# Performance work log

Measured on AMD Instinct MI355X. Metric: run time of the kernel, lower is better.

## Reference

```python
import jax, jax.numpy as jnp
import numpy as np

EMBED_DIM = 1024
NUM_HEADS = 16
HEAD_DIM = EMBED_DIM // NUM_HEADS


def setup_inputs() -> dict:
    key = jax.random.key(0)
    ks = jax.random.split(key, 5)
    B, N, C = 4, 2048, EMBED_DIM
    x = jax.random.normal(ks[0], (B, N, C), dtype=jnp.float32)
    # Linear params (PyTorch layout: weight [out, in])
    s = 1.0 / np.sqrt(C)
    W_qkv = jax.random.uniform(ks[1], (3 * C, C), dtype=jnp.float32, minval=-s, maxval=s)
    b_qkv = jax.random.uniform(ks[2], (3 * C,), dtype=jnp.float32, minval=-s, maxval=s)
    W_out = jax.random.uniform(ks[3], (C, C), dtype=jnp.float32, minval=-s, maxval=s)
    b_out = jax.random.uniform(ks[4], (C,), dtype=jnp.float32, minval=-s, maxval=s)
    return {"x": x, "W_qkv": W_qkv, "b_qkv": b_qkv, "W_out": W_out, "b_out": b_out}


def _rotate_half(t):
    t1, t2 = jnp.split(t, 2, axis=-1)
    return jnp.concatenate((-t2, t1), axis=-1)


def _rope_cos_sin(seq_len, dim, dtype):
    inv_freq = 1.0 / (10000.0 ** (jnp.arange(0, dim, 2, dtype=jnp.float32) / dim))
    t = jnp.arange(seq_len, dtype=jnp.float32)
    freqs = jnp.einsum("i,j->ij", t, inv_freq)  # [N, dim/2]
    emb = jnp.concatenate((freqs, freqs), axis=-1)  # [N, dim]
    return emb.astype(dtype)


def reference(x, W_qkv, b_qkv, W_out, b_out):
    B, N, C = x.shape
    H, D = NUM_HEADS, HEAD_DIM
    qkv = x @ W_qkv.T + b_qkv  # [B, N, 3C]
    qkv = qkv.reshape(B, N, 3, H, D).transpose(2, 0, 3, 1, 4)  # [3, B, H, N, D]
    q, k, v = qkv[0], qkv[1], qkv[2]
    emb = _rope_cos_sin(N, D, x.dtype)
    cos = jnp.cos(emb)[None, None, :, :]  # [1,1,N,D]
    sin = jnp.sin(emb)[None, None, :, :]
    q = q * cos + _rotate_half(q) * sin
    k = k * cos + _rotate_half(k) * sin
    scale = D ** -0.5
    attn = jnp.einsum("bhnd,bhmd->bhnm", q, k) * scale  # [B,H,N,N]
    attn = jax.nn.softmax(attn, axis=-1)
    out = jnp.einsum("bhnm,bhmd->bhnd", attn, v)  # [B,H,N,D]
    out = out.transpose(0, 2, 1, 3).reshape(B, N, C)
    return out @ W_out.T + b_out
```

## Files before the change

### kernel.cpp

```cpp
#include <hip/hip_runtime.h>
#include <hip/hip_bf16.h>
#include <cstdint>
#include <cstddef>

#define SEQ 2048
#define NBATCH 4
#define EMB 1024
#define NH 16
#define HD 64
#define MTOT (NBATCH * SEQ)

typedef __attribute__((ext_vector_type(8))) short bf16x8;
typedef __attribute__((ext_vector_type(4))) float f32x4;
typedef __attribute__((ext_vector_type(16))) float f32x16;
typedef unsigned short u16;
typedef unsigned int u32;

__device__ __forceinline__ float bf2f(u16 v) {
  union { u32 u; float f; } c; c.u = ((u32)v) << 16; return c.f;
}
__device__ __forceinline__ u16 f2bf(float f) {
  union { float f; u32 u; } c; c.f = f;
  u32 u = c.u;
  return (u16)((u + 0x7FFFu + ((u >> 16) & 1u)) >> 16);
}

__global__ void cast_kernel(const float* __restrict__ in, u16* __restrict__ out, int n4) {
  int stride = gridDim.x * blockDim.x;
  for (int i = blockIdx.x * blockDim.x + threadIdx.x; i < n4; i += stride) {
    float4 v = reinterpret_cast<const float4*>(in)[i];
    ushort4 o;
    o.x = f2bf(v.x); o.y = f2bf(v.y); o.z = f2bf(v.z); o.w = f2bf(v.w);
    reinterpret_cast<ushort4*>(out)[i] = o;
  }
}

__global__ void rope_table_kernel(float* __restrict__ tab) {
  int i = blockIdx.x * blockDim.x + threadIdx.x;
  if (i >= SEQ * 32) return;
  int n = i >> 5, j = i & 31;
  float invf = 1.0f / powf(10000.0f, (float)(2 * j) / 64.0f);
  float ang = (float)n * invf;
  tab[i] = cosf(ang);
  tab[SEQ * 32 + i] = sinf(ang);
}

__device__ __forceinline__ void gld_lds16(const u16* g, u16* l) {
  __builtin_amdgcn_global_load_lds((const __attribute__((address_space(1))) void*)g,
                                   (__attribute__((address_space(3))) void*)l, 16, 0, 0);
}

template<bool OUT_F32>
__global__ __launch_bounds__(256, 2)
void gemm_bt(const u16* __restrict__ A, const u16* __restrict__ Bw,
             const float* __restrict__ bias, void* __restrict__ Cout,
             int N, int tiles_n) {
  __shared__ u16 lA[128 * 64];
  __shared__ u16 lB[128 * 64];
  const int K = 1024;
  int bm = blockIdx.x / tiles_n;
  int bn = blockIdx.x % tiles_n;
  int t = threadIdx.x;
  int wave = t >> 6, lane = t & 63;
  int wm = wave >> 1, wn = wave & 1;
  int l15 = lane & 15, l4 = lane >> 4;

  f32x4 acc[4][4];
#pragma unroll
  for (int i = 0; i < 4; ++i)
#pragma unroll
    for (int j = 0; j < 4; ++j) acc[i][j] = (f32x4){0.f, 0.f, 0.f, 0.f};

  int su[4], sr[4], sc[4];
#pragma unroll
  for (int i = 0; i < 4; ++i) {
    int u = (i * 4 + wave) * 64 + lane;
    su[i] = u;
    sr[i] = u >> 3;
    sc[i] = (u & 7) ^ (sr[i] & 7);
  }

  for (int kt = 0; kt < K / 64; ++kt) {
    if (kt) __syncthreads();
#pragma unroll
    for (int i = 0; i < 4; ++i) {
      gld_lds16(A + (size_t)(bm * 128 + sr[i]) * K + kt * 64 + sc[i] * 8, &lA[su[i] * 8]);
      gld_lds16(Bw + (size_t)(bn * 128 + sr[i]) * K + kt * 64 + sc[i] * 8, &lB[su[i] * 8]);
    }
    __syncthreads();
#pragma unroll
    for (int ks = 0; ks < 2; ++ks) {
      bf16x8 af[4], bfr[4];
#pragma unroll
      for (int mb = 0; mb < 4; ++mb) {
        int r = wm * 64 + mb * 16 + l15;
        int cc = (ks * 4 + l4) ^ (r & 7);
        af[mb] = *reinterpret_cast<const bf16x8*>(&lA[r * 64 + cc * 8]);
      }
#pragma unroll
      for (int nb = 0; nb < 4; ++nb) {
        int r = wn * 64 + nb * 16 + l15;
        int cc = (ks * 4 + l4) ^ (r & 7);
        bfr[nb] = *reinterpret_cast<const bf16x8*>(&lB[r * 64 + cc * 8]);
      }
#pragma unroll
      for (int mb = 0; mb < 4; ++mb)
#pragma unroll
        for (int nb = 0; nb < 4; ++nb)
          acc[mb][nb] = __builtin_amdgcn_mfma_f32_16x16x32_bf16(af[mb], bfr[nb], acc[mb][nb], 0, 0, 0);
    }
  }

#pragma unroll
  for (int mb = 0; mb < 4; ++mb)
#pragma unroll
    for (int nb = 0; nb < 4; ++nb) {
      int row0 = bm * 128 + wm * 64 + mb * 16 + l4 * 4;
      int col = bn * 128 + wn * 64 + nb * 16 + l15;
      float bv = bias[col];
#pragma unroll
      for (int r = 0; r < 4; ++r) {
        float v = acc[mb][nb][r] + bv;
        if (OUT_F32)
          reinterpret_cast<float*>(Cout)[(size_t)(row0 + r) * N + col] = v;
        else
          reinterpret_cast<u16*>(Cout)[(size_t)(row0 + r) * N + col] = f2bf(v);
      }
    }
}

__global__ __launch_bounds__(256)
void rope_scatter(const u16* __restrict__ qkv, const float* __restrict__ tab,
                  u16* __restrict__ Q, u16* __restrict__ Kk, u16* __restrict__ Vt) {
  int blk = blockIdx.x;
  int bh = blk >> 5;
  int nt = blk & 31;
  int b = bh >> 4, h = bh & 15;
  int t = threadIdx.x;
  __shared__ u16 vtile[64][72];
  const float* ct = tab;
  const float* st = tab + SEQ * 32;
#pragma unroll
  for (int p = 0; p < 2; ++p) {
    int u = p * 256 + t;
    int r = u >> 3, g = u & 7;
    int n = nt * 64 + r;
    size_t base = (size_t)(b * SEQ + n) * 3072;
    int d0 = g * 8;
    int f0 = d0 & 31;
    bf16x8 qv = *reinterpret_cast<const bf16x8*>(&qkv[base + h * 64 + d0]);
    bf16x8 qp = *reinterpret_cast<const bf16x8*>(&qkv[base + h * 64 + (d0 ^ 32)]);
    bf16x8 kv = *reinterpret_cast<const bf16x8*>(&qkv[base + 1024 + h * 64 + d0]);
    bf16x8 kp = *reinterpret_cast<const bf16x8*>(&qkv[base + 1024 + h * 64 + (d0 ^ 32)]);
    bf16x8 vv = *reinterpret_cast<const bf16x8*>(&qkv[base + 2048 + h * 64 + d0]);
    float4 c0 = *reinterpret_cast<const float4*>(&ct[n * 32 + f0]);
    float4 c1 = *reinterpret_cast<const float4*>(&ct[n * 32 + f0 + 4]);
    float4 s0 = *reinterpret_cast<const float4*>(&st[n * 32 + f0]);
    float4 s1 = *reinterpret_cast<const float4*>(&st[n * 32 + f0 + 4]);
    float sgn = (d0 < 32) ? -1.0f : 1.0f;
    float cs[8] = {c0.x, c0.y, c0.z, c0.w, c1.x, c1.y, c1.z, c1.w};
    float sn[8] = {s0.x, s0.y, s0.z, s0.w, s1.x, s1.y, s1.z, s1.w};
    bf16x8 qo, ko;
#pragma unroll
    for (int j = 0; j < 8; ++j) {
      float qr = bf2f((u16)qv[j]) * cs[j] + sgn * bf2f((u16)qp[j]) * sn[j];
      float kr = bf2f((u16)kv[j]) * cs[j] + sgn * bf2f((u16)kp[j]) * sn[j];
      qo[j] = (short)f2bf(qr * 0.1803368801111163f);
      ko[j] = (short)f2bf(kr);
      vtile[d0 + j][r] = (u16)vv[j];
    }
    size_t qbase = ((size_t)bh * SEQ + n) * 64 + d0;
    *reinterpret_cast<bf16x8*>(&Q[qbase]) = qo;
    *reinterpret_cast<bf16x8*>(&Kk[qbase]) = ko;
  }
  __syncthreads();
#pragma unroll
  for (int p = 0; p < 2; ++p) {
    int u = p * 256 + t;
    int d = u >> 3, c = u & 7;
    bf16x8 o = *reinterpret_cast<const bf16x8*>(&vtile[d][c * 8]);
    *reinterpret_cast<bf16x8*>(&Vt[((size_t)bh * 64 + d) * SEQ + nt * 64 + c * 8]) = o;
  }
}

__global__ __launch_bounds__(256, 2)
void attn_kernel(const u16* __restrict__ Q, const u16* __restrict__ Kk,
                 const u16* __restrict__ Vt, u16* __restrict__ Out) {
  int bid = blockIdx.x;
  int swz = (bid & 7) * 64 + (bid >> 3);
  int bh = swz >> 3;
  int qt = swz & 7;
  int b = bh >> 4, h = bh & 15;
  int t = threadIdx.x;
  int wave = t >> 6, lane = t & 63;
  int l31 = lane & 31, hi = lane >> 5;

  __shared__ u16 lK[2][64 * 64];
  __shared__ u16 lV[2][64 * 64];

  const u16* Qh = Q + (size_t)bh * SEQ * 64;
  const u16* Kh = Kk + (size_t)bh * SEQ * 64;
  const u16* Vh = Vt + (size_t)bh * 64 * SEQ;
  int q0w = qt * 256 + wave * 64;

  bf16x8 qf[2][4];
#pragma unroll
  for (int qb = 0; qb < 2; ++qb)
#pragma unroll
    for (int dc = 0; dc < 4; ++dc)
      qf[qb][dc] = *reinterpret_cast<const bf16x8*>(
          &Qh[(size_t)(q0w + qb * 32 + l31) * 64 + dc * 16 + hi * 8]);

  f32x16 oacc[2][2];
#pragma unroll
  for (int qb = 0; qb < 2; ++qb)
#pragma unroll
    for (int db = 0; db < 2; ++db)
#pragma unroll
      for (int r = 0; r < 16; ++r) oacc[qb][db][r] = 0.f;
  float dn[2] = {0.f, 0.f};

  auto stage = [&](int buf, int kt) {
#pragma unroll
    for (int p = 0; p < 2; ++p) {
      int u = p * 256 + t;
      int r = u >> 3;
      int c = (u & 7) ^ (r & 7);
      gld_lds16(Kh + (size_t)(kt * 64 + r) * 64 + c * 8, &lK[buf][u * 8]);
      gld_lds16(Vh + (size_t)r * SEQ + kt * 64 + c * 8, &lV[buf][u * 8]);
    }
  };

  union PF { u32 w[4]; bf16x8 v; };
  int cur = 0;
  stage(0, 0);
  for (int kt = 0; kt < SEQ / 64; ++kt) {
    if (kt + 1 < SEQ / 64) {
      stage(cur ^ 1, kt + 1);
      asm volatile("s_waitcnt vmcnt(4)" ::: "memory");
    } else {
      asm volatile("s_waitcnt vmcnt(0)" ::: "memory");
    }
    __builtin_amdgcn_s_barrier();

    f32x16 s[2][2];
#pragma unroll
    for (int qb = 0; qb < 2; ++qb)
#pragma unroll
      for (int cb = 0; cb < 2; ++cb)
#pragma unroll
        for (int r = 0; r < 16; ++r) s[qb][cb][r] = 0.f;
#pragma unroll
    for (int cb = 0; cb < 2; ++cb) {
      int krow = cb * 32 + l31;
#pragma unroll
      for (int dc = 0; dc < 4; ++dc) {
        int ch = (dc * 2 + hi) ^ (l31 & 7);
        bf16x8 kf = *reinterpret_cast<const bf16x8*>(&lK[cur][krow * 64 + ch * 8]);
        s[0][cb] = __builtin_amdgcn_mfma_f32_32x32x16_bf16(kf, qf[0][dc], s[0][cb], 0, 0, 0);
        s[1][cb] = __builtin_amdgcn_mfma_f32_32x32x16_bf16(kf, qf[1][dc], s[1][cb], 0, 0, 0);
      }
    }

    PF pa[2][2][2];
#pragma unroll
    for (int qb = 0; qb < 2; ++qb)
#pragma unroll
      for (int cb = 0; cb < 2; ++cb) {
#pragma unroll
        for (int r = 0; r < 16; ++r) {
          float e = __builtin_amdgcn_exp2f(s[qb][cb][r]);
          s[qb][cb][r] = e;
          dn[qb] += e;
        }
#pragma unroll
        for (int c = 0; c < 2; ++c) {
          u32 a1, a2, b1, b2;
          asm("v_cvt_pk_bf16_f32 %0, %1, %2" : "=v"(a1) : "v"(s[qb][cb][8 * c + 0]), "v"(s[qb][cb][8 * c + 1]));
          asm("v_cvt_pk_bf16_f32 %0, %1, %2" : "=v"(a2) : "v"(s[qb][cb][8 * c + 2]), "v"(s[qb][cb][8 * c + 3]));
          asm("v_cvt_pk_bf16_f32 %0, %1, %2" : "=v"(b1) : "v"(s[qb][cb][8 * c + 4]), "v"(s[qb][cb][8 * c + 5]));
          asm("v_cvt_pk_bf16_f32 %0, %1, %2" : "=v"(b2) : "v"(s[qb][cb][8 * c + 6]), "v"(s[qb][cb][8 * c + 7]));
          asm("v_permlane32_swap_b32 %0, %1" : "+v"(a1), "+v"(b1));
          asm("v_permlane32_swap_b32 %0, %1" : "+v"(a2), "+v"(b2));
          pa[qb][cb][c].w[0] = a1; pa[qb][cb][c].w[1] = a2;
          pa[qb][cb][c].w[2] = b1; pa[qb][cb][c].w[3] = b2;
        }
      }

#pragma unroll
    for (int cb = 0; cb < 2; ++cb)
#pragma unroll
      for (int c = 0; c < 2; ++c)
#pragma unroll
        for (int db = 0; db < 2; ++db) {
          int vrow = db * 32 + l31;
          int ch = (cb * 4 + c * 2 + hi) ^ (l31 & 7);
          bf16x8 vf = *reinterpret_cast<const bf16x8*>(&lV[cur][vrow * 64 + ch * 8]);
          oacc[0][db] = __builtin_amdgcn_mfma_f32_32x32x16_bf16(pa[0][cb][c].v, vf, oacc[0][db], 0, 0, 0);
          oacc[1][db] = __builtin_amdgcn_mfma_f32_32x32x16_bf16(pa[1][cb][c].v, vf, oacc[1][db], 0, 0, 0);
        }
    __builtin_amdgcn_s_barrier();
    cur ^= 1;
  }

#pragma unroll
  for (int qb = 0; qb < 2; ++qb) dn[qb] += __shfl_xor(dn[qb], 32);
#pragma unroll
  for (int qb = 0; qb < 2; ++qb)
#pragma unroll
    for (int r = 0; r < 16; ++r) {
      int qrel = (r & 3) + 8 * (r >> 2) + 4 * hi;
      float dfull = __shfl(dn[qb], qrel);
      float inv = __builtin_amdgcn_rcpf(dfull);
      int q = q0w + qb * 32 + qrel;
#pragma unroll
      for (int db = 0; db < 2; ++db) {
        int d = db * 32 + l31;
        Out[(size_t)(b * SEQ + q) * EMB + h * 64 + d] = f2bf(oacc[qb][db][r] * inv);
      }
    }
}

extern "C" void kernel_launch(void* const* d_in, const int* in_sizes, int n_in,
                              void* d_out, int out_size, void* d_ws, size_t ws_size,
                              hipStream_t stream) {
  const float* x = (const float*)d_in[0];
  const float* bqkv = (const float*)d_in[2];
  const float* bout = (const float*)d_in[4];
  float* out = (float*)d_out;

  char* ws = (char*)d_ws;
  size_t off = 0;
  auto alloc = [&](size_t bytes) {
    void* p = ws + off;
    off += (bytes + 255) & ~(size_t)255;
    return p;
  };
  u16* xb    = (u16*)alloc((size_t)MTOT * EMB * 2);
  u16* wqkvb = (u16*)alloc((size_t)3 * EMB * EMB * 2);
  u16* woutb = (u16*)alloc((size_t)EMB * EMB * 2);
  u16* qkv   = (u16*)alloc((size_t)MTOT * 3 * EMB * 2);
  u16* Qb    = (u16*)alloc((size_t)64 * SEQ * HD * 2);
  u16* Kb    = (u16*)alloc((size_t)64 * SEQ * HD * 2);
  u16* Vtb   = (u16*)alloc((size_t)64 * HD * SEQ * 2);
  u16* aout  = (u16*)alloc((size_t)MTOT * EMB * 2);
  float* tab = (float*)alloc((size_t)2 * SEQ * 32 * 4);
  (void)ws_size; (void)in_sizes; (void)n_in; (void)out_size;

  cast_kernel<<<2048, 256, 0, stream>>>(x, xb, MTOT * EMB / 4);
  cast_kernel<<<1024, 256, 0, stream>>>((const float*)d_in[1], wqkvb, 3 * EMB * EMB / 4);
  cast_kernel<<<512, 256, 0, stream>>>((const float*)d_in[3], woutb, EMB * EMB / 4);
  rope_table_kernel<<<(SEQ * 32 + 255) / 256, 256, 0, stream>>>(tab);

  gemm_bt<false><<<64 * 24, 256, 0, stream>>>(xb, wqkvb, bqkv, qkv, 3 * EMB, 24);
  rope_scatter<<<64 * 32, 256, 0, stream>>>(qkv, tab, Qb, Kb, Vtb);
  attn_kernel<<<64 * 8, 256, 0, stream>>>(Qb, Kb, Vtb, aout);
  gemm_bt<true><<<64 * 8, 256, 0, stream>>>(aout, woutb, bout, out, EMB, 8);
}
```

Measured before the change: 190.1 us.

## Halve per-wave query tile in attention to double blocks and occupancy

The attention kernel now gives each wave 32 query rows instead of 64, so each block covers 128 queries, the grid doubles to 1024 blocks and launch bounds rise to 4 blocks per SM. The aim is to cut register pressure and raise occupancy and parallelism so MFMA and exp latency are hidden better. The cost is that every K/V tile is staged into LDS twice as often relative to the compute done on it. It also replaces the packed v_cvt_pk_bf16_f32 asm with software rounding via f2bf, which adds ALU instructions per element.

```diff
diff --git a/kernel.cpp b/kernel.cpp
--- a/kernel.cpp
+++ b/kernel.cpp
@@ -183,13 +183,13 @@
   }
 }
 
-__global__ __launch_bounds__(256, 2)
+__global__ __launch_bounds__(256, 4)
 void attn_kernel(const u16* __restrict__ Q, const u16* __restrict__ Kk,
                  const u16* __restrict__ Vt, u16* __restrict__ Out) {
   int bid = blockIdx.x;
-  int swz = (bid & 7) * 64 + (bid >> 3);
-  int bh = swz >> 3;
-  int qt = swz & 7;
+  int swz = (bid & 7) * 128 + (bid >> 3);
+  int bh = swz >> 4;
+  int qt = swz & 15;
   int b = bh >> 4, h = bh & 15;
   int t = threadIdx.x;
   int wave = t >> 6, lane = t & 63;
@@ -201,24 +201,20 @@
   const u16* Qh = Q + (size_t)bh * SEQ * 64;
   const u16* Kh = Kk + (size_t)bh * SEQ * 64;
   const u16* Vh = Vt + (size_t)bh * 64 * SEQ;
-  int q0w = qt * 256 + wave * 64;
-
-  bf16x8 qf[2][4];
-#pragma unroll
-  for (int qb = 0; qb < 2; ++qb)
-#pragma unroll
-    for (int dc = 0; dc < 4; ++dc)
-      qf[qb][dc] = *reinterpret_cast<const bf16x8*>(
-          &Qh[(size_t)(q0w + qb * 32 + l31) * 64 + dc * 16 + hi * 8]);
-
-  f32x16 oacc[2][2];
-#pragma unroll
-  for (int qb = 0; qb < 2; ++qb)
-#pragma unroll
-    for (int db = 0; db < 2; ++db)
-#pragma unroll
-      for (int r = 0; r < 16; ++r) oacc[qb][db][r] = 0.f;
-  float dn[2] = {0.f, 0.f};
+  int q0w = qt * 128 + wave * 32;
+
+  bf16x8 qf[4];
+#pragma unroll
+  for (int dc = 0; dc < 4; ++dc)
+    qf[dc] = *reinterpret_cast<const bf16x8*>(
+        &Qh[(size_t)(q0w + l31) * 64 + dc * 16 + hi * 8]);
+
+  f32x16 oacc[2];
+#pragma unroll
+  for (int db = 0; db < 2; ++db)
+#pragma unroll
+    for (int r = 0; r < 16; ++r) oacc[db][r] = 0.f;
+  float dn = 0.f;
 
   auto stage = [&](int buf, int kt) {
 #pragma unroll
@@ -243,13 +239,11 @@
     }
     __builtin_amdgcn_s_barrier();
 
-    f32x16 s[2][2];
-#pragma unroll
-    for (int qb = 0; qb < 2; ++qb)
-#pragma unroll
-      for (int cb = 0; cb < 2; ++cb)
-#pragma unroll
-        for (int r = 0; r < 16; ++r) s[qb][cb][r] = 0.f;
+    f32x16 s[2];
+#pragma unroll
+    for (int cb = 0; cb < 2; ++cb)
+#pragma unroll
+      for (int r = 0; r < 16; ++r) s[cb][r] = 0.f;
 #pragma unroll
     for (int cb = 0; cb < 2; ++cb) {
       int krow = cb * 32 + l31;
@@ -257,35 +251,33 @@
       for (int dc = 0; dc < 4; ++dc) {
         int ch = (dc * 2 + hi) ^ (l31 & 7);
         bf16x8 kf = *reinterpret_cast<const bf16x8*>(&lK[cur][krow * 64 + ch * 8]);
-        s[0][cb] = __builtin_amdgcn_mfma_f32_32x32x16_bf16(kf, qf[0][dc], s[0][cb], 0, 0, 0);
-        s[1][cb] = __builtin_amdgcn_mfma_f32_32x32x16_bf16(kf, qf[1][dc], s[1][cb], 0, 0, 0);
-      }
-    }
-
-    PF pa[2][2][2];
-#pragma unroll
-    for (int qb = 0; qb < 2; ++qb)
-#pragma unroll
-      for (int cb = 0; cb < 2; ++cb) {
-#pragma unroll
-        for (int r = 0; r < 16; ++r) {
-          float e = __builtin_amdgcn_exp2f(s[qb][cb][r]);
-          s[qb][cb][r] = e;
-          dn[qb] += e;
-        }
-#pragma unroll
-        for (int c = 0; c < 2; ++c) {
-          u32 a1, a2, b1, b2;
-          asm("v_cvt_pk_bf16_f32 %0, %1, %2" : "=v"(a1) : "v"(s[qb][cb][8 * c + 0]), "v"(s[qb][cb][8 * c + 1]));
-          asm("v_cvt_pk_bf16_f32 %0, %1, %2" : "=v"(a2) : "v"(s[qb][cb][8 * c + 2]), "v"(s[qb][cb][8 * c + 3]));
-          asm("v_cvt_pk_bf16_f32 %0, %1, %2" : "=v"(b1) : "v"(s[qb][cb][8 * c + 4]), "v"(s[qb][cb][8 * c + 5]));
-          asm("v_cvt_pk_bf16_f32 %0, %1, %2" : "=v"(b2) : "v"(s[qb][cb][8 * c + 6]), "v"(s[qb][cb][8 * c + 7]));
-          asm("v_permlane32_swap_b32 %0, %1" : "+v"(a1), "+v"(b1));
-          asm("v_permlane32_swap_b32 %0, %1" : "+v"(a2), "+v"(b2));
-          pa[qb][cb][c].w[0] = a1; pa[qb][cb][c].w[1] = a2;
-          pa[qb][cb][c].w[2] = b1; pa[qb][cb][c].w[3] = b2;
-        }
-      }
+        s[cb] = __builtin_amdgcn_mfma_f32_32x32x16_bf16(kf, qf[dc], s[cb], 0, 0, 0);
+      }
+    }
+
+    PF pa[2][2];
+#pragma unroll
+    for (int cb = 0; cb < 2; ++cb) {
+#pragma unroll
+      for (int r = 0; r < 16; ++r) {
+        float e = __builtin_amdgcn_exp2f(s[cb][r]);
+        s[cb][r] = e;
+        dn += e;
+      }
+#pragma unroll
+      for (int c = 0; c < 2; ++c) {
+        u32 r0 = f2bf(s[cb][8 * c + 0]), r1 = f2bf(s[cb][8 * c + 1]);
+        u32 r2 = f2bf(s[cb][8 * c + 2]), r3 = f2bf(s[cb][8 * c + 3]);
+        u32 r4 = f2bf(s[cb][8 * c + 4]), r5 = f2bf(s[cb][8 * c + 5]);
+        u32 r6 = f2bf(s[cb][8 * c + 6]), r7 = f2bf(s[cb][8 * c + 7]);
+        u32 a1 = r0 | (r1 << 16), a2 = r2 | (r3 << 16);
+        u32 b1 = r4 | (r5 << 16), b2 = r6 | (r7 << 16);
+        asm("v_permlane32_swap_b32 %0, %1" : "+v"(a1), "+v"(b1));
+        asm("v_permlane32_swap_b32 %0, %1" : "+v"(a2), "+v"(b2));
+        pa[cb][c].w[0] = a1; pa[cb][c].w[1] = a2;
+        pa[cb][c].w[2] = b1; pa[cb][c].w[3] = b2;
+      }
+    }
 
 #pragma unroll
     for (int cb = 0; cb < 2; ++cb)
@@ -296,29 +288,25 @@
           int vrow = db * 32 + l31;
           int ch = (cb * 4 + c * 2 + hi) ^ (l31 & 7);
           bf16x8 vf = *reinterpret_cast<const bf16x8*>(&lV[cur][vrow * 64 + ch * 8]);
-          oacc[0][db] = __builtin_amdgcn_mfma_f32_32x32x16_bf16(pa[0][cb][c].v, vf, oacc[0][db], 0, 0, 0);
-          oacc[1][db] = __builtin_amdgcn_mfma_f32_32x32x16_bf16(pa[1][cb][c].v, vf, oacc[1][db], 0, 0, 0);
+          oacc[db] = __builtin_amdgcn_mfma_f32_32x32x16_bf16(pa[cb][c].v, vf, oacc[db], 0, 0, 0);
         }
     __builtin_amdgcn_s_barrier();
     cur ^= 1;
   }
 
-#pragma unroll
-  for (int qb = 0; qb < 2; ++qb) dn[qb] += __shfl_xor(dn[qb], 32);
-#pragma unroll
-  for (int qb = 0; qb < 2; ++qb)
-#pragma unroll
-    for (int r = 0; r < 16; ++r) {
-      int qrel = (r & 3) + 8 * (r >> 2) + 4 * hi;
-      float dfull = __shfl(dn[qb], qrel);
-      float inv = __builtin_amdgcn_rcpf(dfull);
-      int q = q0w + qb * 32 + qrel;
-#pragma unroll
-      for (int db = 0; db < 2; ++db) {
-        int d = db * 32 + l31;
-        Out[(size_t)(b * SEQ + q) * EMB + h * 64 + d] = f2bf(oacc[qb][db][r] * inv);
-      }
-    }
+  dn += __shfl_xor(dn, 32);
+#pragma unroll
+  for (int r = 0; r < 16; ++r) {
+    int qrel = (r & 3) + 8 * (r >> 2) + 4 * hi;
+    float dfull = __shfl(dn, qrel);
+    float inv = __builtin_amdgcn_rcpf(dfull);
+    int q = q0w + qrel;
+#pragma unroll
+    for (int db = 0; db < 2; ++db) {
+      int d = db * 32 + l31;
+      Out[(size_t)(b * SEQ + q) * EMB + h * 64 + d] = f2bf(oacc[db][r] * inv);
+    }
+  }
 }
 
 extern "C" void kernel_launch(void* const* d_in, const int* in_sizes, int n_in,
@@ -354,6 +342,6 @@
 
   gemm_bt<false><<<64 * 24, 256, 0, stream>>>(xb, wqkvb, bqkv, qkv, 3 * EMB, 24);
   rope_scatter<<<64 * 32, 256, 0, stream>>>(qkv, tab, Qb, Kb, Vtb);
-  attn_kernel<<<64 * 8, 256, 0, stream>>>(Qb, Kb, Vtb, aout);
+  attn_kernel<<<64 * 16, 256, 0, stream>>>(Qb, Kb, Vtb, aout);
   gemm_bt<true><<<64 * 8, 256, 0, stream>>>(aout, woutb, bout, out, EMB, 8);
 }
```

New measurement: 208.4 us. +9.6%, slower.
